# Optimization experiments

Measured on AMD Instinct MI355X. Metric: run time of the kernel, lower is better.

The kernel has to match this reference:

```python
import jax, jax.numpy as jnp
import numpy as np

HIDDEN = 128
INT_EMB = 64
NUM_SPH = 7
E = 262144
T = 2097152


def _glorot(key, shape):
    fan_in, fan_out = shape[1], shape[0]
    limit = np.sqrt(6.0 / (fan_in + fan_out))
    return jax.random.uniform(key, shape, jnp.float32, -limit, limit)


def setup_inputs() -> dict:
    key = jax.random.key(0)
    ks = jax.random.split(key, 10)
    edge_attr = jax.random.normal(ks[0], (E, HIDDEN), jnp.float32)
    sbf = jax.random.normal(ks[1], (T, NUM_SPH), jnp.float32)
    idx_kj = jax.random.randint(ks[2], (T,), 0, E)
    idx_ji = jax.random.randint(ks[3], (T,), 0, E)
    # Linear weights stored torch-style as [out_features, in_features]
    W_sbf0 = _glorot(ks[4], (NUM_SPH, NUM_SPH))
    W_sbf = _glorot(ks[5], (INT_EMB, NUM_SPH))
    W_e1 = _glorot(ks[6], (HIDDEN, 2 * HIDDEN))
    b_e1 = jnp.zeros((HIDDEN,), jnp.float32)
    W_down = _glorot(ks[7], (INT_EMB, HIDDEN))
    W_up = _glorot(ks[8], (HIDDEN, INT_EMB))
    return {
        "edge_attr": edge_attr, "sbf": sbf, "idx_kj": idx_kj, "idx_ji": idx_ji,
        "W_sbf0": W_sbf0, "W_sbf": W_sbf, "W_e1": W_e1, "b_e1": b_e1,
        "W_down": W_down, "W_up": W_up,
    }


def reference(edge_attr, sbf, idx_kj, idx_ji, W_sbf0, W_sbf, W_e1, b_e1, W_down, W_up):
    act = jax.nn.silu
    # x = act(lin_down(edge_attr))  [E, INT_EMB]
    x = act(edge_attr @ W_down.T)
    # sbf basis projections [T, INT_EMB]
    s = (sbf @ W_sbf0.T) @ W_sbf.T
    # gather by idx_kj, modulate, scatter-add onto idx_ji
    m = x[idx_kj] * s                                   # [T, INT_EMB]
    agg = jax.ops.segment_sum(m, idx_ji, num_segments=edge_attr.shape[0])
    # up-project and edge update
    u = act(agg @ W_up.T)                               # [E, HIDDEN]
    h = act(jnp.concatenate([edge_attr, u], axis=-1) @ W_e1.T + b_e1)
    return h + edge_attr
```

## Files before the change

### kernel.cpp

```cpp
#include <hip/hip_runtime.h>
#include <hip/hip_bf16.h>

#define NSPH 7

typedef short bf16x8 __attribute__((ext_vector_type(8)));
typedef float f32x4 __attribute__((ext_vector_type(4)));

static __device__ __forceinline__ ushort f2b(float f) {
    union { __hip_bfloat16 h; ushort u; } v; v.h = __float2bfloat16(f); return v.u;
}
static __device__ __forceinline__ float b2f(ushort u) {
    union { unsigned int i; float f; } v; v.i = ((unsigned int)u) << 16; return v.f;
}
static __device__ __forceinline__ float silu_f(float v) {
    return v / (1.0f + __expf(-v));
}
static __device__ __forceinline__ bf16x8 ld8_f32_to_bf16(const float* p) {
    float4 p0 = *(const float4*)p;
    float4 p1 = *(const float4*)(p + 4);
    bf16x8 r;
    r[0] = (short)f2b(p0.x); r[1] = (short)f2b(p0.y);
    r[2] = (short)f2b(p0.z); r[3] = (short)f2b(p0.w);
    r[4] = (short)f2b(p1.x); r[5] = (short)f2b(p1.y);
    r[6] = (short)f2b(p1.z); r[7] = (short)f2b(p1.w);
    return r;
}

__launch_bounds__(256)
__global__ void k1_down(const float* __restrict__ edge, const float* __restrict__ Wd,
                        ushort* __restrict__ X) {
    const int tid  = threadIdx.x;
    const int lane = tid & 63;
    const int w    = tid >> 6;
    const int quad = lane >> 4;
    const int m16  = lane & 15;
    const int r0   = blockIdx.x * 128 + w * 32;

    f32x4 acc[2][4];
#pragma unroll
    for (int mi = 0; mi < 2; mi++)
#pragma unroll
        for (int ni = 0; ni < 4; ni++) acc[mi][ni] = (f32x4){0.f, 0.f, 0.f, 0.f};

#pragma unroll
    for (int k = 0; k < 128; k += 32) {
        bf16x8 a[2], b[4];
#pragma unroll
        for (int mi = 0; mi < 2; mi++)
            a[mi] = ld8_f32_to_bf16(&edge[(size_t)(r0 + mi * 16 + m16) * 128 + k + quad * 8]);
#pragma unroll
        for (int ni = 0; ni < 4; ni++)
            b[ni] = ld8_f32_to_bf16(&Wd[(ni * 16 + m16) * 128 + k + quad * 8]);
#pragma unroll
        for (int mi = 0; mi < 2; mi++)
#pragma unroll
            for (int ni = 0; ni < 4; ni++)
                acc[mi][ni] = __builtin_amdgcn_mfma_f32_16x16x32_bf16(a[mi], b[ni], acc[mi][ni], 0, 0, 0);
    }
#pragma unroll
    for (int mi = 0; mi < 2; mi++)
#pragma unroll
        for (int ni = 0; ni < 4; ni++)
#pragma unroll
            for (int r = 0; r < 4; r++) {
                int row = r0 + mi * 16 + quad * 4 + r;
                int col = ni * 16 + m16;
                X[(size_t)row * 64 + col] = f2b(silu_f(acc[mi][ni][r]));
            }
}

__launch_bounds__(256)
__global__ void k2_scatter(const int* __restrict__ kj, const int* __restrict__ ji,
                           const float* __restrict__ sbf, const ushort* __restrict__ X,
                           const float* __restrict__ Wsbf, const float* __restrict__ Wsbf0,
                           float* agg_out, int T) {
    const int lane = threadIdx.x & 63;
    float wj[NSPH], wc[NSPH];
#pragma unroll
    for (int i = 0; i < NSPH; i++) wj[i] = Wsbf[lane * NSPH + i];
#pragma unroll
    for (int k = 0; k < NSPH; k++) {
        float a = 0.f;
#pragma unroll
        for (int i = 0; i < NSPH; i++) a += wj[i] * Wsbf0[i * NSPH + k];
        wc[k] = a;
    }
    int gw = (blockIdx.x * 256 + threadIdx.x) >> 6;
    int nw = (gridDim.x * 256) >> 6;
    for (int t = gw; t < T; t += nw) {
        int a = kj[t];
        int b = ji[t];
        float s = 0.f;
#pragma unroll
        for (int k = 0; k < NSPH; k++) s += wc[k] * sbf[(size_t)t * NSPH + k];
        float val = b2f(X[(size_t)a * 64 + lane]) * s;
        unsafeAtomicAdd(&agg_out[(size_t)b * 128 + lane], val);
    }
}

__launch_bounds__(256)
__global__ void k3_fused(const float* __restrict__ edge, const float* __restrict__ Wu,
                         const float* __restrict__ We, const float* __restrict__ bias,
                         float* out) {
    __shared__ __align__(16) short Ut[128 * 136];
    const int tid  = threadIdx.x;
    const int lane = tid & 63;
    const int w    = tid >> 6;
    const int quad = lane >> 4;
    const int m16  = lane & 15;
    const int r0   = blockIdx.x * 128;
    const int rowbase = (w >> 1) * 64;
    const int colbase = (w & 1) * 64;

    f32x4 acc1[4][4];
#pragma unroll
    for (int mi = 0; mi < 4; mi++)
#pragma unroll
        for (int ni = 0; ni < 4; ni++) acc1[mi][ni] = (f32x4){0.f, 0.f, 0.f, 0.f};

#pragma unroll
    for (int kk = 0; kk < 64; kk += 32) {
        bf16x8 a[4], b[4];
#pragma unroll
        for (int mi = 0; mi < 4; mi++)
            a[mi] = ld8_f32_to_bf16(&out[(size_t)(r0 + rowbase + mi * 16 + m16) * 128 + kk + quad * 8]);
#pragma unroll
        for (int ni = 0; ni < 4; ni++)
            b[ni] = ld8_f32_to_bf16(&Wu[(colbase + ni * 16 + m16) * 64 + kk + quad * 8]);
#pragma unroll
        for (int mi = 0; mi < 4; mi++)
#pragma unroll
            for (int ni = 0; ni < 4; ni++)
                acc1[mi][ni] = __builtin_amdgcn_mfma_f32_16x16x32_bf16(a[mi], b[ni], acc1[mi][ni], 0, 0, 0);
    }
#pragma unroll
    for (int mi = 0; mi < 4; mi++)
#pragma unroll
        for (int ni = 0; ni < 4; ni++)
#pragma unroll
            for (int r = 0; r < 4; r++) {
                int rl = rowbase + mi * 16 + quad * 4 + r;
                int cl = colbase + ni * 16 + m16;
                Ut[rl * 136 + cl] = (short)f2b(silu_f(acc1[mi][ni][r]));
            }
    __syncthreads();

    f32x4 acc2[4][4];
#pragma unroll
    for (int mi = 0; mi < 4; mi++)
#pragma unroll
        for (int ni = 0; ni < 4; ni++) acc2[mi][ni] = (f32x4){0.f, 0.f, 0.f, 0.f};

#pragma unroll
    for (int k = 0; k < 256; k += 32) {
        bf16x8 a[4], b[4];
#pragma unroll
        for (int mi = 0; mi < 4; mi++) {
            int rl = rowbase + mi * 16 + m16;
            if (k < 128)
                a[mi] = ld8_f32_to_bf16(&edge[(size_t)(r0 + rl) * 128 + k + quad * 8]);
            else
                a[mi] = *(const bf16x8*)&Ut[rl * 136 + (k - 128) + quad * 8];
        }
#pragma unroll
        for (int ni = 0; ni < 4; ni++)
            b[ni] = ld8_f32_to_bf16(&We[(size_t)(colbase + ni * 16 + m16) * 256 + k + quad * 8]);
#pragma unroll
        for (int mi = 0; mi < 4; mi++)
#pragma unroll
            for (int ni = 0; ni < 4; ni++)
                acc2[mi][ni] = __builtin_amdgcn_mfma_f32_16x16x32_bf16(a[mi], b[ni], acc2[mi][ni], 0, 0, 0);
    }

#pragma unroll
    for (int mi = 0; mi < 4; mi++)
#pragma unroll
        for (int ni = 0; ni < 4; ni++) {
            int col = colbase + ni * 16 + m16;
            float bcol = bias[col];
#pragma unroll
            for (int r = 0; r < 4; r++) {
                int row = r0 + rowbase + mi * 16 + quad * 4 + r;
                float pre = acc2[mi][ni][r] + bcol;
                out[(size_t)row * 128 + col] = silu_f(pre) + edge[(size_t)row * 128 + col];
            }
        }
}

extern "C" void kernel_launch(void* const* d_in, const int* in_sizes, int n_in,
                              void* d_out, int out_size, void* d_ws, size_t ws_size,
                              hipStream_t stream) {
    const float* edge  = (const float*)d_in[0];
    const float* sbf   = (const float*)d_in[1];
    const int*   idxkj = (const int*)d_in[2];
    const int*   idxji = (const int*)d_in[3];
    const float* Wsbf0 = (const float*)d_in[4];
    const float* Wsbf  = (const float*)d_in[5];
    const float* We1   = (const float*)d_in[6];
    const float* be1   = (const float*)d_in[7];
    const float* Wdown = (const float*)d_in[8];
    const float* Wup   = (const float*)d_in[9];

    const int E = in_sizes[0] / 128;
    const int T = in_sizes[2];

    ushort* X   = (ushort*)d_ws;
    float*  out = (float*)d_out;

    hipMemsetAsync(d_out, 0, (size_t)out_size * sizeof(float), stream);
    k1_down<<<E / 128, 256, 0, stream>>>(edge, Wdown, X);
    k2_scatter<<<8192, 256, 0, stream>>>(idxkj, idxji, sbf, X, Wsbf, Wsbf0, out, T);
    k3_fused<<<E / 128, 256, 0, stream>>>(edge, Wup, We1, be1, out);
}
```

Measured before the change: 948.3 us.

## Replace atomic scatter-add with counting-sort by destination and segmented reduction

```diff
diff --git a/kernel.cpp b/kernel.cpp
--- a/kernel.cpp
+++ b/kernel.cpp
@@ -70,10 +70,77 @@
 }
 
 __launch_bounds__(256)
-__global__ void k2_scatter(const int* __restrict__ kj, const int* __restrict__ ji,
-                           const float* __restrict__ sbf, const ushort* __restrict__ X,
-                           const float* __restrict__ Wsbf, const float* __restrict__ Wsbf0,
-                           float* agg_out, int T) {
+__global__ void k_hist(const int* __restrict__ ji, int* __restrict__ counts, int T) {
+    int i = blockIdx.x * 256 + threadIdx.x;
+    int n = gridDim.x * 256;
+    for (int t = i; t < T; t += n) atomicAdd(&counts[ji[t]], 1);
+}
+
+__launch_bounds__(256)
+__global__ void k_scan_bsum(const int* __restrict__ counts, int* __restrict__ bsum) {
+    __shared__ int sm[256];
+    int tid = threadIdx.x;
+    sm[tid] = counts[blockIdx.x * 256 + tid];
+    __syncthreads();
+#pragma unroll
+    for (int off = 128; off > 0; off >>= 1) {
+        if (tid < off) sm[tid] += sm[tid + off];
+        __syncthreads();
+    }
+    if (tid == 0) bsum[blockIdx.x] = sm[0];
+}
+
+__launch_bounds__(1024)
+__global__ void k_scan_top(int* __restrict__ bsum, int NB) {
+    __shared__ int sm[1024];
+    int tid = threadIdx.x;
+    int v = (tid < NB) ? bsum[tid] : 0;
+    sm[tid] = v;
+    __syncthreads();
+    for (int off = 1; off < 1024; off <<= 1) {
+        int x = (tid >= off) ? sm[tid - off] : 0;
+        __syncthreads();
+        sm[tid] += x;
+        __syncthreads();
+    }
+    if (tid < NB) bsum[tid] = sm[tid] - v;
+}
+
+__launch_bounds__(256)
+__global__ void k_scan_down(const int* __restrict__ counts, const int* __restrict__ bsum,
+                            int* __restrict__ offsets) {
+    __shared__ int sm[256];
+    int tid = threadIdx.x;
+    int g = blockIdx.x * 256 + tid;
+    int v = counts[g];
+    sm[tid] = v;
+    __syncthreads();
+    for (int off = 1; off < 256; off <<= 1) {
+        int x = (tid >= off) ? sm[tid - off] : 0;
+        __syncthreads();
+        sm[tid] += x;
+        __syncthreads();
+    }
+    offsets[g] = bsum[blockIdx.x] + sm[tid] - v;
+}
+
+__launch_bounds__(256)
+__global__ void k_scatter_idx(const int* __restrict__ ji, int* __restrict__ cursor,
+                              int* __restrict__ perm, int T) {
+    int i = blockIdx.x * 256 + threadIdx.x;
+    int n = gridDim.x * 256;
+    for (int t = i; t < T; t += n) {
+        int pos = atomicAdd(&cursor[ji[t]], 1);
+        perm[pos] = t;
+    }
+}
+
+__launch_bounds__(256)
+__global__ void k2_seg(const int* __restrict__ kj, const int* __restrict__ perm,
+                       const int* __restrict__ counts, const int* __restrict__ ends,
+                       const float* __restrict__ sbf, const ushort* __restrict__ X,
+                       const float* __restrict__ Wsbf, const float* __restrict__ Wsbf0,
+                       float* __restrict__ out, int E) {
     const int lane = threadIdx.x & 63;
     float wj[NSPH], wc[NSPH];
 #pragma unroll
@@ -87,14 +154,21 @@
     }
     int gw = (blockIdx.x * 256 + threadIdx.x) >> 6;
     int nw = (gridDim.x * 256) >> 6;
-    for (int t = gw; t < T; t += nw) {
-        int a = kj[t];
-        int b = ji[t];
-        float s = 0.f;
-#pragma unroll
-        for (int k = 0; k < NSPH; k++) s += wc[k] * sbf[(size_t)t * NSPH + k];
-        float val = b2f(X[(size_t)a * 64 + lane]) * s;
-        unsafeAtomicAdd(&agg_out[(size_t)b * 128 + lane], val);
+    for (int r = gw; r < E; r += nw) {
+        int rs  = __builtin_amdgcn_readfirstlane(r);
+        int c   = counts[rs];
+        int end = ends[rs];
+        int st  = end - c;
+        float acc = 0.f;
+        for (int i = 0; i < c; i++) {
+            int t = __builtin_amdgcn_readfirstlane(perm[st + i]);
+            int a = kj[t];
+            float s = 0.f;
+#pragma unroll
+            for (int k = 0; k < NSPH; k++) s += wc[k] * sbf[(size_t)t * NSPH + k];
+            acc += b2f(X[(size_t)a * 64 + lane]) * s;
+        }
+        out[(size_t)rs * 128 + lane] = acc;
     }
 }
 
@@ -203,12 +277,28 @@
 
     const int E = in_sizes[0] / 128;
     const int T = in_sizes[2];
-
-    ushort* X   = (ushort*)d_ws;
-    float*  out = (float*)d_out;
-
-    hipMemsetAsync(d_out, 0, (size_t)out_size * sizeof(float), stream);
+    const int NB = E / 256;
+
+    ushort* X       = (ushort*)d_ws;
+    int*    counts  = (int*)((char*)d_ws + (size_t)E * 64 * 2);
+    int*    offsets = counts + E;
+    int*    perm    = offsets + E;
+    int*    bsum    = perm + T;
+
+    float* out = (float*)d_out;
+
+    hipMemsetAsync(counts, 0, (size_t)E * sizeof(int), stream);
+
     k1_down<<<E / 128, 256, 0, stream>>>(edge, Wdown, X);
-    k2_scatter<<<8192, 256, 0, stream>>>(idxkj, idxji, sbf, X, Wsbf, Wsbf0, out, T);
+
+    k_hist<<<2048, 256, 0, stream>>>(idxji, counts, T);
+    k_scan_bsum<<<NB, 256, 0, stream>>>(counts, bsum);
+    k_scan_top<<<1, 1024, 0, stream>>>(bsum, NB);
+    k_scan_down<<<NB, 256, 0, stream>>>(counts, bsum, offsets);
+    k_scatter_idx<<<2048, 256, 0, stream>>>(idxji, offsets, perm, T);
+
+    k2_seg<<<4096, 256, 0, stream>>>(idxkj, perm, counts, offsets, sbf, X,
+                                     Wsbf, Wsbf0, out, E);
+
     k3_fused<<<E / 128, 256, 0, stream>>>(edge, Wup, We1, be1, out);
 }
```

After: 1.110 ms. +17.0%, slower.
